# Kernel optimization log

Measured on AMD Instinct MI355X. Metric: run time of the kernel, lower is better.

## Reference

```python
import jax, jax.numpy as jnp
import numpy as np

EMBED_DIM = 256
NUM_HEADS = 8
HEAD_DIM = EMBED_DIM // NUM_HEADS
LN_EPS = 1e-5


def _linear_init(key, fan_in, fan_out):
    # torch nn.Linear default: U(-1/sqrt(fan_in), 1/sqrt(fan_in)) for W and b
    kw, kb = jax.random.split(key)
    bound = 1.0 / np.sqrt(fan_in)
    W = jax.random.uniform(kw, (fan_out, fan_in), jnp.float32, -bound, bound)
    b = jax.random.uniform(kb, (fan_out,), jnp.float32, -bound, bound)
    return W, b


def setup_inputs() -> dict:
    key = jax.random.key(0)
    ks = jax.random.split(key, 6)
    x = jax.random.normal(ks[0], (2, 512, EMBED_DIM), jnp.float32)
    Wq, bq = _linear_init(ks[1], EMBED_DIM, EMBED_DIM)
    Wk, bk = _linear_init(ks[2], EMBED_DIM, EMBED_DIM)
    Wv, bv = _linear_init(ks[3], EMBED_DIM, EMBED_DIM)
    Wr, br = _linear_init(ks[4], EMBED_DIM, EMBED_DIM)
    Wo, bo = _linear_init(ks[5], EMBED_DIM, EMBED_DIM)
    g1 = jnp.ones((EMBED_DIM,), jnp.float32)
    b1 = jnp.zeros((EMBED_DIM,), jnp.float32)
    g2 = jnp.ones((EMBED_DIM,), jnp.float32)
    b2 = jnp.zeros((EMBED_DIM,), jnp.float32)
    return {"x": x, "Wq": Wq, "bq": bq, "Wk": Wk, "bk": bk, "Wv": Wv, "bv": bv,
            "Wr": Wr, "br": br, "Wo": Wo, "bo": bo,
            "g1": g1, "b1": b1, "g2": g2, "b2": b2}


def _layer_norm(x, g, b):
    mu = jnp.mean(x, axis=-1, keepdims=True)
    var = jnp.mean(jnp.square(x - mu), axis=-1, keepdims=True)
    return (x - mu) * jax.lax.rsqrt(var + LN_EPS) * g + b


def reference(x, Wq, bq, Wk, bk, Wv, bv, Wr, br, Wo, bo, g1, b1, g2, b2):
    B, N, D = x.shape
    H, Dh = NUM_HEADS, HEAD_DIM
    Q = x @ Wq.T + bq  # [B,N,D]
    K = x @ Wk.T + bk
    V = x @ Wv.T + bv
    # pairwise differences, projected: [B,N,N,D]
    R = x[:, :, None, :] - x[:, None, :, :]
    R = jnp.einsum('bijd,ed->bije', R, Wr) + br
    max_R1 = jnp.max(R, axis=1)  # [B,N,D] (max over rows -> bias for Q)
    max_R2 = jnp.max(R, axis=2)  # [B,N,D] (max over cols -> bias for K)
    Q_r = Q + max_R1
    K_r = K + max_R2
    # [B,H,N,Dh]
    Q_r = Q_r.reshape(B, N, H, Dh).transpose(0, 2, 1, 3)
    K_r = K_r.reshape(B, N, H, Dh).transpose(0, 2, 1, 3)
    Vh = V.reshape(B, N, H, Dh).transpose(0, 2, 1, 3)
    scores = jnp.einsum('bhqd,bhkd->bhqk', Q_r, K_r) / np.sqrt(Dh).astype(np.float32)
    probs = jax.nn.softmax(scores, axis=-1)
    attn = jnp.einsum('bhqk,bhkd->bhqd', probs, Vh)
    attn = attn.transpose(0, 2, 1, 3).reshape(B, N, D)
    attn = attn @ Wo.T + bo  # dropout is identity in eval mode
    h = _layer_norm(x + attn, g1, b1)
    return _layer_norm(h, g2, b2)
```

## Files before the change

### kernel.cpp

```cpp
#include <hip/hip_runtime.h>
#include <hip/hip_bf16.h>
#include <math.h>

#define NSEQ 512
#define EMB 256

typedef __attribute__((ext_vector_type(8))) short bf16x8;
typedef __attribute__((ext_vector_type(4))) float f32x4;

__device__ __forceinline__ unsigned short f2bf(float f) {
    unsigned u = __float_as_uint(f);
    unsigned r = (u + 0x7FFFu + ((u >> 16) & 1u)) >> 16;
    return (unsigned short)r;
}
__device__ __forceinline__ float bf2f(unsigned short s) {
    return __uint_as_float(((unsigned)s) << 16);
}
__device__ __forceinline__ ushort4 cvt4(float4 v) {
    ushort4 o;
    o.x = f2bf(v.x); o.y = f2bf(v.y); o.z = f2bf(v.z); o.w = f2bf(v.w);
    return o;
}

__global__ __launch_bounds__(256) void k_gemm_mfma(
    const float* __restrict__ X,
    const float* __restrict__ Wq, const float* __restrict__ Wk,
    const float* __restrict__ Wv, const float* __restrict__ Wr,
    const float* __restrict__ Wo,
    const float* __restrict__ bq, const float* __restrict__ bv,
    unsigned short* __restrict__ Qb, unsigned short* __restrict__ Kb,
    unsigned short* __restrict__ Vtb, unsigned short* __restrict__ Wob,
    float* __restrict__ maxPart)
{
    const int t = threadIdx.x;

    if (blockIdx.y == 16) {
        const float4* Wg = (const float4*)Wo;
        #pragma unroll
        for (int i = 0; i < 4; ++i) {
            int idx4 = blockIdx.x * 1024 + i * 256 + t;
            ((ushort4*)Wob)[idx4] = cvt4(Wg[idx4]);
        }
        return;
    }

    __shared__ __align__(16) unsigned short Xs[64 * 264];
    __shared__ __align__(16) unsigned short Ws[64 * 264];
    __shared__ float red[4][64];

    const int w = t >> 6, l = t & 63;
    const int ln = l & 15, kg = l >> 4;
    const int m0 = blockIdx.x * 64;
    const int nW = blockIdx.y * 64;
    const int seg = blockIdx.y >> 2;
    const int wbase = (blockIdx.y & 3) * 64;

    const float4* X4  = (const float4*)X;
    const float4* Wq4 = (const float4*)Wq;
    const float4* Wk4 = (const float4*)Wk;
    const float4* Wv4 = (const float4*)Wv;
    const float4* Wr4 = (const float4*)Wr;

    #pragma unroll
    for (int i = 0; i < 16; ++i) {
        int idx = i * 256 + t;
        int row = idx >> 6, c4 = idx & 63;
        float4 xv = X4[(size_t)(m0 + row) * 64 + c4];
        *(ushort4*)(Xs + row * 264 + c4 * 4) = cvt4(xv);

        size_t off = (size_t)(wbase + row) * 64 + c4;
        float4 wv;
        if (seg == 0) {
            float4 a = Wq4[off], r = Wr4[off];
            wv = make_float4(a.x - r.x, a.y - r.y, a.z - r.z, a.w - r.w);
        } else if (seg == 1) {
            float4 a = Wk4[off], r = Wr4[off];
            wv = make_float4(a.x + r.x, a.y + r.y, a.z + r.z, a.w + r.w);
        } else if (seg == 2) {
            wv = Wv4[off];
        } else {
            wv = Wr4[off];
        }
        *(ushort4*)(Ws + row * 264 + c4 * 4) = cvt4(wv);
    }
    __syncthreads();

    f32x4 acc[4] = {{0.f,0.f,0.f,0.f},{0.f,0.f,0.f,0.f},
                    {0.f,0.f,0.f,0.f},{0.f,0.f,0.f,0.f}};
    const int arow = (w << 4) + ln;
    #pragma unroll
    for (int ks = 0; ks < 8; ++ks) {
        bf16x8 a = *(const bf16x8*)(Xs + arow * 264 + ks * 32 + kg * 8);
        #pragma unroll
        for (int nf = 0; nf < 4; ++nf) {
            bf16x8 b = *(const bf16x8*)(Ws + (nf * 16 + ln) * 264 + ks * 32 + kg * 8);
            acc[nf] = __builtin_amdgcn_mfma_f32_16x16x32_bf16(a, b, acc[nf], 0, 0, 0);
        }
    }

    if (seg == 0) {
        #pragma unroll
        for (int nf = 0; nf < 4; ++nf) {
            int c = (nW & 255) + nf * 16 + ln;
            float bb = bq[c];
            #pragma unroll
            for (int r = 0; r < 4; ++r) {
                int row = m0 + w * 16 + kg * 4 + r;
                Qb[(size_t)row * 256 + c] = f2bf(acc[nf][r] + bb);
            }
        }
    } else if (seg == 1) {
        #pragma unroll
        for (int nf = 0; nf < 4; ++nf) {
            int c = (nW & 255) + nf * 16 + ln;
            #pragma unroll
            for (int r = 0; r < 4; ++r) {
                int row = m0 + w * 16 + kg * 4 + r;
                Kb[(size_t)row * 256 + c] = f2bf(acc[nf][r]);
            }
        }
    } else if (seg == 2) {
        #pragma unroll
        for (int nf = 0; nf < 4; ++nf) {
            int c = (nW & 255) + nf * 16 + ln;
            int h = c >> 5, d = c & 31;
            float bb = bv[c];
            #pragma unroll
            for (int r = 0; r < 4; ++r) {
                int row = m0 + w * 16 + kg * 4 + r;
                int b = row >> 9, ml = row & 511;
                Vtb[((size_t)(b * 8 + h) * 32 + d) * 512 + ml] = f2bf(acc[nf][r] + bb);
            }
        }
    } else {
        #pragma unroll
        for (int nf = 0; nf < 4; ++nf) {
            float mx = fmaxf(fmaxf(acc[nf][0], acc[nf][1]),
                             fmaxf(acc[nf][2], acc[nf][3]));
            mx = fmaxf(mx, __shfl_xor(mx, 16));
            mx = fmaxf(mx, __shfl_xor(mx, 32));
            if (l < 16) red[w][nf * 16 + ln] = mx;
        }
        __syncthreads();
        if (t < 64) {
            float m = fmaxf(fmaxf(red[0][t], red[1][t]),
                            fmaxf(red[2][t], red[3][t]));
            const int b = blockIdx.x >> 3;
            const int mblk = blockIdx.x & 7;
            maxPart[b * 2048 + mblk * 256 + (nW & 255) + t] = m;
        }
    }
}

__global__ __launch_bounds__(256) void k_attn_mfma(
    const unsigned short* __restrict__ Qb,
    const unsigned short* __restrict__ Kb,
    const unsigned short* __restrict__ Vtb,
    const float* __restrict__ maxPart,
    const float* __restrict__ br,
    unsigned short* __restrict__ attnb)
{
    __shared__ __align__(16) unsigned short Plds[4][16][136];
    __shared__ float Olds[4][16][33];
    __shared__ float mlds[4][16], llds[4][16];
    __shared__ float scl[4][16], Li[16];
    __shared__ float qadd[32];

    const int t = threadIdx.x;
    const int w = t >> 6, l = t & 63;
    const int ln = l & 15, kg = l >> 4;
    const int q0 = blockIdx.x * 16;
    const int h = blockIdx.y, b = blockIdx.z;
    const int e0 = h * 32;
    const int bh = b * 8 + h;
    const float scale = 0.17677669529663687f;

    if (t < 32) {
        float m = maxPart[b * 2048 + e0 + t];
        #pragma unroll
        for (int j = 1; j < 8; ++j)
            m = fmaxf(m, maxPart[b * 2048 + j * 256 + e0 + t]);
        qadd[t] = m + br[e0 + t];
    }
    __syncthreads();

    bf16x8 af;
    {
        size_t qrow = (size_t)(b * NSEQ + q0 + ln) * 256 + e0 + kg * 8;
        bf16x8 qa = *(const bf16x8*)(Qb + qrow);
        #pragma unroll
        for (int j = 0; j < 8; ++j) {
            int d = kg * 8 + j;
            float qv = bf2f((unsigned short)qa[j]);
            af[j] = (short)f2bf((qv + qadd[d]) * scale);
        }
    }

    const int key0 = w * 128;
    f32x4 sc[8];
    #pragma unroll
    for (int kf = 0; kf < 8; ++kf) {
        size_t krow = (size_t)(b * NSEQ + key0 + kf * 16 + ln) * 256 + e0 + kg * 8;
        bf16x8 bfr = *(const bf16x8*)(Kb + krow);
        f32x4 z = {0.f, 0.f, 0.f, 0.f};
        sc[kf] = __builtin_amdgcn_mfma_f32_16x16x32_bf16(af, bfr, z, 0, 0, 0);
    }

    float m_[4], l_[4];
    #pragma unroll
    for (int r = 0; r < 4; ++r) {
        float mx = sc[0][r];
        #pragma unroll
        for (int kf = 1; kf < 8; ++kf) mx = fmaxf(mx, sc[kf][r]);
        #pragma unroll
        for (int off = 1; off < 16; off <<= 1) mx = fmaxf(mx, __shfl_xor(mx, off));
        m_[r] = mx;
        float s = 0.f;
        #pragma unroll
        for (int kf = 0; kf < 8; ++kf) {
            float p = __expf(sc[kf][r] - mx);
            sc[kf][r] = p;
            s += p;
        }
        #pragma unroll
        for (int off = 1; off < 16; off <<= 1) s += __shfl_xor(s, off);
        l_[r] = s;
    }

    #pragma unroll
    for (int kf = 0; kf < 8; ++kf)
        #pragma unroll
        for (int r = 0; r < 4; ++r)
            Plds[w][kg * 4 + r][kf * 16 + ln] = f2bf(sc[kf][r]);

    f32x4 o[2] = {{0.f,0.f,0.f,0.f},{0.f,0.f,0.f,0.f}};
    #pragma unroll
    for (int ks = 0; ks < 4; ++ks) {
        bf16x8 pf = *(const bf16x8*)&Plds[w][ln][ks * 32 + kg * 8];
        #pragma unroll
        for (int df = 0; df < 2; ++df) {
            size_t vrow = ((size_t)bh * 32 + df * 16 + ln) * 512 + key0 + ks * 32 + kg * 8;
            bf16x8 vf = *(const bf16x8*)(Vtb + vrow);
            o[df] = __builtin_amdgcn_mfma_f32_16x16x32_bf16(pf, vf, o[df], 0, 0, 0);
        }
    }

    if (ln == 0) {
        #pragma unroll
        for (int r = 0; r < 4; ++r) {
            mlds[w][kg * 4 + r] = m_[r];
            llds[w][kg * 4 + r] = l_[r];
        }
    }
    #pragma unroll
    for (int df = 0; df < 2; ++df)
        #pragma unroll
        for (int r = 0; r < 4; ++r)
            Olds[w][kg * 4 + r][df * 16 + ln] = o[df][r];
    __syncthreads();

    if (t < 16) {
        float M = fmaxf(fmaxf(mlds[0][t], mlds[1][t]),
                        fmaxf(mlds[2][t], mlds[3][t]));
        float L = 0.f;
        #pragma unroll
        for (int wv = 0; wv < 4; ++wv) {
            float s = __expf(mlds[wv][t] - M);
            scl[wv][t] = s;
            L += s * llds[wv][t];
        }
        Li[t] = 1.f / L;
    }
    __syncthreads();

    #pragma unroll
    for (int i = 0; i < 2; ++i) {
        int idx = t + 256 * i;
        int q = idx >> 5, d = idx & 31;
        float acc = 0.f;
        #pragma unroll
        for (int wv = 0; wv < 4; ++wv)
            acc += scl[wv][q] * Olds[wv][q][d];
        attnb[(size_t)(b * NSEQ + q0 + q) * 256 + e0 + d] = f2bf(acc * Li[q]);
    }
}

__global__ __launch_bounds__(256) void k_ogemm_mfma(
    const unsigned short* __restrict__ Ab,
    const unsigned short* __restrict__ Wob,
    float* __restrict__ yPart)
{
    __shared__ __align__(16) unsigned short As_[64 * 72];
    __shared__ __align__(16) unsigned short Bs_[64 * 72];

    const int t = threadIdx.x;
    const int w = t >> 6, l = t & 63;
    const int ln = l & 15, kg = l >> 4;
    const int m0 = blockIdx.x * 64;
    const int n0 = blockIdx.y * 64;
    const int bz = blockIdx.z;

    const uint4* Ag = (const uint4*)Ab;
    const uint4* Wg = (const uint4*)Wob;
    #pragma unroll
    for (int i = 0; i < 2; ++i) {
        int idx = i * 256 + t;
        int row = idx >> 3, c8 = idx & 7;
        *(uint4*)(As_ + row * 72 + c8 * 8) = Ag[(size_t)(m0 + row) * 32 + bz * 8 + c8];
        *(uint4*)(Bs_ + row * 72 + c8 * 8) = Wg[(size_t)(n0 + row) * 32 + bz * 8 + c8];
    }
    __syncthreads();

    f32x4 acc[4] = {{0.f,0.f,0.f,0.f},{0.f,0.f,0.f,0.f},
                    {0.f,0.f,0.f,0.f},{0.f,0.f,0.f,0.f}};
    const int arow = (w << 4) + ln;
    #pragma unroll
    for (int ks = 0; ks < 2; ++ks) {
        bf16x8 a = *(const bf16x8*)(As_ + arow * 72 + ks * 32 + kg * 8);
        #pragma unroll
        for (int nf = 0; nf < 4; ++nf) {
            bf16x8 b = *(const bf16x8*)(Bs_ + (nf * 16 + ln) * 72 + ks * 32 + kg * 8);
            acc[nf] = __builtin_amdgcn_mfma_f32_16x16x32_bf16(a, b, acc[nf], 0, 0, 0);
        }
    }

    float* dst = yPart + (size_t)bz * (1024 * 256);
    #pragma unroll
    for (int nf = 0; nf < 4; ++nf) {
        #pragma unroll
        for (int r = 0; r < 4; ++r) {
            int row = m0 + w * 16 + kg * 4 + r;
            dst[(size_t)row * 256 + n0 + nf * 16 + ln] = acc[nf][r];
        }
    }
}

__global__ __launch_bounds__(256) void k_lnorm(
    const float* __restrict__ yP, const float* __restrict__ x,
    const float* __restrict__ bo,
    const float* __restrict__ g1, const float* __restrict__ b1,
    const float* __restrict__ g2, const float* __restrict__ b2,
    float* __restrict__ out)
{
    __shared__ float red[4][4][2];
    const int t = threadIdx.x;
    const int r0 = blockIdx.x * 4;
    const int c = t;
    const int wid = t >> 6, lane = t & 63;

    float y[4];
    #pragma unroll
    for (int r = 0; r < 4; ++r) {
        size_t off = (size_t)(r0 + r) * 256 + c;
        y[r] = x[off] + bo[c] + yP[off] + yP[262144 + off]
             + yP[524288 + off] + yP[786432 + off];
    }

    #pragma unroll
    for (int r = 0; r < 4; ++r) {
        float s = y[r], s2 = y[r] * y[r];
        #pragma unroll
        for (int off = 32; off > 0; off >>= 1) {
            s  += __shfl_xor(s, off);
            s2 += __shfl_xor(s2, off);
        }
        if (lane == 0) { red[wid][r][0] = s; red[wid][r][1] = s2; }
    }
    __syncthreads();
    float t1[4];
    #pragma unroll
    for (int r = 0; r < 4; ++r) {
        float s  = red[0][r][0] + red[1][r][0] + red[2][r][0] + red[3][r][0];
        float s2 = red[0][r][1] + red[1][r][1] + red[2][r][1] + red[3][r][1];
        float mu = s * (1.f / 256.f);
        float var = s2 * (1.f / 256.f) - mu * mu;
        float rs = rsqrtf(var + 1e-5f);
        t1[r] = (y[r] - mu) * rs * g1[c] + b1[c];
    }
    __syncthreads();

    #pragma unroll
    for (int r = 0; r < 4; ++r) {
        float s = t1[r], s2 = t1[r] * t1[r];
        #pragma unroll
        for (int off = 32; off > 0; off >>= 1) {
            s  += __shfl_xor(s, off);
            s2 += __shfl_xor(s2, off);
        }
        if (lane == 0) { red[wid][r][0] = s; red[wid][r][1] = s2; }
    }
    __syncthreads();
    #pragma unroll
    for (int r = 0; r < 4; ++r) {
        float s  = red[0][r][0] + red[1][r][0] + red[2][r][0] + red[3][r][0];
        float s2 = red[0][r][1] + red[1][r][1] + red[2][r][1] + red[3][r][1];
        float mu = s * (1.f / 256.f);
        float var = s2 * (1.f / 256.f) - mu * mu;
        float rs = rsqrtf(var + 1e-5f);
        out[(size_t)(r0 + r) * 256 + c] = (t1[r] - mu) * rs * g2[c] + b2[c];
    }
}

extern "C" void kernel_launch(void* const* d_in, const int* in_sizes, int n_in,
                              void* d_out, int out_size, void* d_ws, size_t ws_size,
                              hipStream_t stream)
{
    const float* x  = (const float*)d_in[0];
    const float* Wq = (const float*)d_in[1];
    const float* bq = (const float*)d_in[2];
    const float* Wk = (const float*)d_in[3];
    const float* bk = (const float*)d_in[4];
    const float* Wv = (const float*)d_in[5];
    const float* bv = (const float*)d_in[6];
    const float* Wr = (const float*)d_in[7];
    const float* br = (const float*)d_in[8];
    const float* Wo = (const float*)d_in[9];
    const float* bo = (const float*)d_in[10];
    const float* g1 = (const float*)d_in[11];
    const float* b1 = (const float*)d_in[12];
    const float* g2 = (const float*)d_in[13];
    const float* b2 = (const float*)d_in[14];
    float* out = (float*)d_out;
    (void)bk;

    unsigned short* u = (unsigned short*)d_ws;
    unsigned short* Qb    = u;
    unsigned short* Kb    = u + 262144;
    unsigned short* Vtb   = u + 524288;
    unsigned short* attnb = u + 786432;
    unsigned short* Wob   = u + 1048576;
    float* maxPart = (float*)(u + 1114112);
    float* yP      = (float*)(u + 1122304);

    k_gemm_mfma<<<dim3(16, 17), 256, 0, stream>>>(x, Wq, Wk, Wv, Wr, Wo, bq, bv,
                                                  Qb, Kb, Vtb, Wob, maxPart);
    k_attn_mfma<<<dim3(32, 8, 2), 256, 0, stream>>>(Qb, Kb, Vtb, maxPart, br, attnb);
    k_ogemm_mfma<<<dim3(16, 4, 4), 256, 0, stream>>>(attnb, Wob, yP);
    k_lnorm<<<256, 256, 0, stream>>>(yP, x, bo, g1, b1, g2, b2, out);
}
```

Measured before the change: 28.34 us.

## Process 32 queries per attention block and store split-K partials as bf16

Each attention workgroup now covers two 16-query fragments, so every K and V fragment loaded from global memory feeds two MFMAs, and the grid shrinks from 512 to 256 blocks. Separately, the split-K output projection now writes its partial sums as bf16 instead of fp32, which halves the bytes written by the GEMM and read by the layernorm kernel. The costs are higher register and LDS use per attention block, fewer blocks to spread across CUs, and extra rounding error in the summed partials.

After: 27.10 us. 4.4% less time.

```diff
diff --git a/kernel.cpp b/kernel.cpp
--- a/kernel.cpp
+++ b/kernel.cpp
@@ -160,106 +160,122 @@
     const float* __restrict__ br,
     unsigned short* __restrict__ attnb)
 {
-    __shared__ __align__(16) unsigned short Plds[4][16][136];
-    __shared__ float Olds[4][16][33];
-    __shared__ float mlds[4][16], llds[4][16];
-    __shared__ float scl[4][16], Li[16];
+    __shared__ __align__(16) unsigned short Plds[4][32][136];
+    __shared__ float Olds[4][32][33];
+    __shared__ float mlds[4][32], llds[4][32];
+    __shared__ float scl[4][32], Li[32];
     __shared__ float qadd[32];
 
     const int t = threadIdx.x;
     const int w = t >> 6, l = t & 63;
     const int ln = l & 15, kg = l >> 4;
-    const int q0 = blockIdx.x * 16;
-    const int h = blockIdx.y, b = blockIdx.z;
+    const int q0 = blockIdx.x * 32;
+    const int h = blockIdx.y, bz = blockIdx.z;
     const int e0 = h * 32;
-    const int bh = b * 8 + h;
+    const int bh = bz * 8 + h;
     const float scale = 0.17677669529663687f;
 
     if (t < 32) {
-        float m = maxPart[b * 2048 + e0 + t];
+        float m = maxPart[bz * 2048 + e0 + t];
         #pragma unroll
         for (int j = 1; j < 8; ++j)
-            m = fmaxf(m, maxPart[b * 2048 + j * 256 + e0 + t]);
+            m = fmaxf(m, maxPart[bz * 2048 + j * 256 + e0 + t]);
         qadd[t] = m + br[e0 + t];
     }
     __syncthreads();
 
-    bf16x8 af;
-    {
-        size_t qrow = (size_t)(b * NSEQ + q0 + ln) * 256 + e0 + kg * 8;
+    bf16x8 af[2];
+    #pragma unroll
+    for (int qf = 0; qf < 2; ++qf) {
+        size_t qrow = (size_t)(bz * NSEQ + q0 + qf * 16 + ln) * 256 + e0 + kg * 8;
         bf16x8 qa = *(const bf16x8*)(Qb + qrow);
         #pragma unroll
         for (int j = 0; j < 8; ++j) {
             int d = kg * 8 + j;
-            float qv = bf2f((unsigned short)qa[j]);
-            af[j] = (short)f2bf((qv + qadd[d]) * scale);
+            af[qf][j] = (short)f2bf((bf2f((unsigned short)qa[j]) + qadd[d]) * scale);
         }
     }
 
     const int key0 = w * 128;
-    f32x4 sc[8];
+    f32x4 sc[2][8];
     #pragma unroll
     for (int kf = 0; kf < 8; ++kf) {
-        size_t krow = (size_t)(b * NSEQ + key0 + kf * 16 + ln) * 256 + e0 + kg * 8;
+        size_t krow = (size_t)(bz * NSEQ + key0 + kf * 16 + ln) * 256 + e0 + kg * 8;
         bf16x8 bfr = *(const bf16x8*)(Kb + krow);
         f32x4 z = {0.f, 0.f, 0.f, 0.f};
-        sc[kf] = __builtin_amdgcn_mfma_f32_16x16x32_bf16(af, bfr, z, 0, 0, 0);
-    }
-
-    float m_[4], l_[4];
-    #pragma unroll
-    for (int r = 0; r < 4; ++r) {
-        float mx = sc[0][r];
-        #pragma unroll
-        for (int kf = 1; kf < 8; ++kf) mx = fmaxf(mx, sc[kf][r]);
-        #pragma unroll
-        for (int off = 1; off < 16; off <<= 1) mx = fmaxf(mx, __shfl_xor(mx, off));
-        m_[r] = mx;
-        float s = 0.f;
-        #pragma unroll
-        for (int kf = 0; kf < 8; ++kf) {
-            float p = __expf(sc[kf][r] - mx);
-            sc[kf][r] = p;
-            s += p;
-        }
-        #pragma unroll
-        for (int off = 1; off < 16; off <<= 1) s += __shfl_xor(s, off);
-        l_[r] = s;
-    }
-
-    #pragma unroll
-    for (int kf = 0; kf < 8; ++kf)
-        #pragma unroll
-        for (int r = 0; r < 4; ++r)
-            Plds[w][kg * 4 + r][kf * 16 + ln] = f2bf(sc[kf][r]);
-
-    f32x4 o[2] = {{0.f,0.f,0.f,0.f},{0.f,0.f,0.f,0.f}};
+        sc[0][kf] = __builtin_amdgcn_mfma_f32_16x16x32_bf16(af[0], bfr, z, 0, 0, 0);
+        sc[1][kf] = __builtin_amdgcn_mfma_f32_16x16x32_bf16(af[1], bfr, z, 0, 0, 0);
+    }
+
+    float m_[2][4], l_[2][4];
+    #pragma unroll
+    for (int qf = 0; qf < 2; ++qf) {
+        #pragma unroll
+        for (int r = 0; r < 4; ++r) {
+            float mx = sc[qf][0][r];
+            #pragma unroll
+            for (int kf = 1; kf < 8; ++kf) mx = fmaxf(mx, sc[qf][kf][r]);
+            #pragma unroll
+            for (int off = 1; off < 16; off <<= 1) mx = fmaxf(mx, __shfl_xor(mx, off));
+            m_[qf][r] = mx;
+            float s = 0.f;
+            #pragma unroll
+            for (int kf = 0; kf < 8; ++kf) {
+                float p = __expf(sc[qf][kf][r] - mx);
+                sc[qf][kf][r] = p;
+                s += p;
+            }
+            #pragma unroll
+            for (int off = 1; off < 16; off <<= 1) s += __shfl_xor(s, off);
+            l_[qf][r] = s;
+        }
+    }
+
+    #pragma unroll
+    for (int qf = 0; qf < 2; ++qf)
+        #pragma unroll
+        for (int kf = 0; kf < 8; ++kf)
+            #pragma unroll
+            for (int r = 0; r < 4; ++r)
+                Plds[w][qf * 16 + kg * 4 + r][kf * 16 + ln] = f2bf(sc[qf][kf][r]);
+
+    f32x4 o[2][2] = {{{0.f,0.f,0.f,0.f},{0.f,0.f,0.f,0.f}},
+                     {{0.f,0.f,0.f,0.f},{0.f,0.f,0.f,0.f}}};
     #pragma unroll
     for (int ks = 0; ks < 4; ++ks) {
-        bf16x8 pf = *(const bf16x8*)&Plds[w][ln][ks * 32 + kg * 8];
+        bf16x8 vf[2];
         #pragma unroll
         for (int df = 0; df < 2; ++df) {
             size_t vrow = ((size_t)bh * 32 + df * 16 + ln) * 512 + key0 + ks * 32 + kg * 8;
-            bf16x8 vf = *(const bf16x8*)(Vtb + vrow);
-            o[df] = __builtin_amdgcn_mfma_f32_16x16x32_bf16(pf, vf, o[df], 0, 0, 0);
+            vf[df] = *(const bf16x8*)(Vtb + vrow);
+        }
+        #pragma unroll
+        for (int qf = 0; qf < 2; ++qf) {
+            bf16x8 pf = *(const bf16x8*)&Plds[w][qf * 16 + ln][ks * 32 + kg * 8];
+            o[qf][0] = __builtin_amdgcn_mfma_f32_16x16x32_bf16(pf, vf[0], o[qf][0], 0, 0, 0);
+            o[qf][1] = __builtin_amdgcn_mfma_f32_16x16x32_bf16(pf, vf[1], o[qf][1], 0, 0, 0);
         }
     }
 
     if (ln == 0) {
         #pragma unroll
-        for (int r = 0; r < 4; ++r) {
-            mlds[w][kg * 4 + r] = m_[r];
-            llds[w][kg * 4 + r] = l_[r];
-        }
-    }
-    #pragma unroll
-    for (int df = 0; df < 2; ++df)
-        #pragma unroll
-        for (int r = 0; r < 4; ++r)
-            Olds[w][kg * 4 + r][df * 16 + ln] = o[df][r];
-    __syncthreads();
-
-    if (t < 16) {
+        for (int qf = 0; qf < 2; ++qf)
+            #pragma unroll
+            for (int r = 0; r < 4; ++r) {
+                mlds[w][qf * 16 + kg * 4 + r] = m_[qf][r];
+                llds[w][qf * 16 + kg * 4 + r] = l_[qf][r];
+            }
+    }
+    #pragma unroll
+    for (int qf = 0; qf < 2; ++qf)
+        #pragma unroll
+        for (int df = 0; df < 2; ++df)
+            #pragma unroll
+            for (int r = 0; r < 4; ++r)
+                Olds[w][qf * 16 + kg * 4 + r][df * 16 + ln] = o[qf][df][r];
+    __syncthreads();
+
+    if (t < 32) {
         float M = fmaxf(fmaxf(mlds[0][t], mlds[1][t]),
                         fmaxf(mlds[2][t], mlds[3][t]));
         float L = 0.f;
@@ -274,21 +290,21 @@
     __syncthreads();
 
     #pragma unroll
-    for (int i = 0; i < 2; ++i) {
+    for (int i = 0; i < 4; ++i) {
         int idx = t + 256 * i;
         int q = idx >> 5, d = idx & 31;
         float acc = 0.f;
         #pragma unroll
         for (int wv = 0; wv < 4; ++wv)
             acc += scl[wv][q] * Olds[wv][q][d];
-        attnb[(size_t)(b * NSEQ + q0 + q) * 256 + e0 + d] = f2bf(acc * Li[q]);
+        attnb[(size_t)(bz * NSEQ + q0 + q) * 256 + e0 + d] = f2bf(acc * Li[q]);
     }
 }
 
 __global__ __launch_bounds__(256) void k_ogemm_mfma(
     const unsigned short* __restrict__ Ab,
     const unsigned short* __restrict__ Wob,
-    float* __restrict__ yPart)
+    unsigned short* __restrict__ yPb)
 {
     __shared__ __align__(16) unsigned short As_[64 * 72];
     __shared__ __align__(16) unsigned short Bs_[64 * 72];
@@ -324,19 +340,19 @@
         }
     }
 
-    float* dst = yPart + (size_t)bz * (1024 * 256);
+    unsigned short* dst = yPb + (size_t)bz * (1024 * 256);
     #pragma unroll
     for (int nf = 0; nf < 4; ++nf) {
         #pragma unroll
         for (int r = 0; r < 4; ++r) {
             int row = m0 + w * 16 + kg * 4 + r;
-            dst[(size_t)row * 256 + n0 + nf * 16 + ln] = acc[nf][r];
+            dst[(size_t)row * 256 + n0 + nf * 16 + ln] = f2bf(acc[nf][r]);
         }
     }
 }
 
 __global__ __launch_bounds__(256) void k_lnorm(
-    const float* __restrict__ yP, const float* __restrict__ x,
+    const unsigned short* __restrict__ yPb, const float* __restrict__ x,
     const float* __restrict__ bo,
     const float* __restrict__ g1, const float* __restrict__ b1,
     const float* __restrict__ g2, const float* __restrict__ b2,
@@ -352,8 +368,9 @@
     #pragma unroll
     for (int r = 0; r < 4; ++r) {
         size_t off = (size_t)(r0 + r) * 256 + c;
-        y[r] = x[off] + bo[c] + yP[off] + yP[262144 + off]
-             + yP[524288 + off] + yP[786432 + off];
+        y[r] = x[off] + bo[c]
+             + bf2f(yPb[off]) + bf2f(yPb[262144 + off])
+             + bf2f(yPb[524288 + off]) + bf2f(yPb[786432 + off]);
     }
 
     #pragma unroll
@@ -430,11 +447,11 @@
     unsigned short* attnb = u + 786432;
     unsigned short* Wob   = u + 1048576;
     float* maxPart = (float*)(u + 1114112);
-    float* yP      = (float*)(u + 1122304);
+    unsigned short* yPb = u + 1122304;
 
     k_gemm_mfma<<<dim3(16, 17), 256, 0, stream>>>(x, Wq, Wk, Wv, Wr, Wo, bq, bv,
                                                   Qb, Kb, Vtb, Wob, maxPart);
-    k_attn_mfma<<<dim3(32, 8, 2), 256, 0, stream>>>(Qb, Kb, Vtb, maxPart, br, attnb);
-    k_ogemm_mfma<<<dim3(16, 4, 4), 256, 0, stream>>>(attnb, Wob, yP);
-    k_lnorm<<<256, 256, 0, stream>>>(yP, x, bo, g1, b1, g2, b2, out);
-}
+    k_attn_mfma<<<dim3(16, 8, 2), 256, 0, stream>>>(Qb, Kb, Vtb, maxPart, br, attnb);
+    k_ogemm_mfma<<<dim3(16, 4, 4), 256, 0, stream>>>(attnb, Wob, yPb);
+    k_lnorm<<<256, 256, 0, stream>>>(yPb, x, bo, g1, b1, g2, b2, out);
+}
```
